# Kernel tuning notes

Hardware: AMD Instinct MI355X
Metric: run time of the kernel (lower is better)

The kernel has to match this reference:

```python
import jax, jax.numpy as jnp
import numpy as np
import math

D_MODEL = 512
N_HEADS = 4
ANCHOR_PERIODS = [12, 24, 48, 96]
MIN_PERIOD = 4


def compute_periods(x, k=2, min_period=MIN_PERIOD):
    # x: [B, T, C] -> per-channel top-k ACF periods [C, k] (torch code runs this under no_grad)
    B, T, C = x.shape
    xc = x - x.mean(axis=1, keepdims=True)
    n_fft = 1 << (2 * T - 1).bit_length()
    xf = jnp.fft.rfft(xc, n=n_fft, axis=1)
    acf = jnp.fft.irfft(xf * jnp.conj(xf), n=n_fft, axis=1)[:, :T, :]
    avg = acf.mean(axis=0)  # [T, C]
    neg = jnp.array(-jnp.inf, avg.dtype)
    avg = avg.at[:min_period, :].set(neg)
    prev = jnp.roll(avg, 1, axis=0)
    nxt = jnp.roll(avg, -1, axis=0)
    is_peak = (avg > prev) & (avg > nxt) & (avg > 0)
    masked = jnp.where(is_peak, avg, neg)
    _, inds = jax.lax.top_k(masked.T, k)  # [C, k], top over lag axis
    return jnp.clip(inds, min_period, T // 2)


def _interp_matrix(new_len, old_len):
    # rows of F.interpolate(eye, size=(new_len, old_len), mode='bilinear', align_corners=False)
    j = np.arange(new_len, dtype=np.float64)
    src = np.clip((j + 0.5) * old_len / new_len - 0.5, 0.0, old_len - 1)
    i0 = np.floor(src).astype(np.int64)
    i1 = np.minimum(i0 + 1, old_len - 1)
    w = src - i0
    M = np.zeros((new_len, old_len), np.float32)
    M[np.arange(new_len), i0] += (1.0 - w).astype(np.float32)
    M[np.arange(new_len), i1] += w.astype(np.float32)
    return M


def flex_weight(anchors, target_len):
    nearest = min(ANCHOR_PERIODS, key=lambda p: abs(p - target_len))
    old = anchors[nearest]  # [d, nearest]
    if nearest == target_len:
        return old
    M = _interp_matrix(target_len, nearest)          # [new, old]
    Mpinv = jnp.asarray(np.linalg.pinv(M.T))          # pinv(resize_mat.T): [new, old]
    return (Mpinv @ old.T).T * math.sqrt(target_len / nearest)  # [d, new]


def attentive_agg(tokens, in_w, in_b, out_w, out_b, ln_g, ln_b):
    # tokens: [N, P, d]; MHA(query=last patch, key=value=all patches), eval mode (dropout=identity)
    N, P, d = tokens.shape
    hd = d // N_HEADS
    q = tokens[:, -1:, :]  # [N, 1, d]
    Wq, Wk, Wv = jnp.split(in_w, 3, axis=0)
    bq, bk, bv = jnp.split(in_b, 3)

    def heads(t, W, b):
        y = t @ W.T + b
        return y.reshape(N, t.shape[1], N_HEADS, hd).transpose(0, 2, 1, 3)

    Q = heads(q, Wq, bq)       # [N, H, 1, hd]
    K = heads(tokens, Wk, bk)  # [N, H, P, hd]
    V = heads(tokens, Wv, bv)
    attn = jax.nn.softmax(jnp.einsum('nhqe,nhke->nhqk', Q, K) / math.sqrt(hd), axis=-1)
    o = jnp.einsum('nhqk,nhke->nhqe', attn, V).transpose(0, 2, 1, 3).reshape(N, 1, d)
    o = o @ out_w.T + out_b
    y = q + o
    mu = y.mean(-1, keepdims=True)
    var = y.var(-1, keepdims=True)
    y = (y - mu) * jax.lax.rsqrt(var + 1e-5) * ln_g + ln_b
    return y[:, 0, :]


def setup_inputs() -> dict:
    key = jax.random.key(0)
    ks = jax.random.split(key, 16)
    B, T, C, d = 16, 384, 128, D_MODEL

    def xavier(k, shape):
        lim = math.sqrt(6.0 / (shape[0] + shape[1]))
        return jax.random.uniform(k, shape, jnp.float32, -lim, lim)

    inp = {'x': jax.random.normal(ks[0], (B, T, C), jnp.float32)}
    for i, p in enumerate(ANCHOR_PERIODS):
        inp[f'anchor_w{p}'] = xavier(ks[1 + i], (d, p))
    inp['shared_bias'] = jnp.zeros((d,), jnp.float32)
    for j, tag in enumerate(['agg1', 'agg2']):
        inp[f'{tag}_in_w'] = xavier(ks[5 + 2 * j], (3 * d, d))
        inp[f'{tag}_in_b'] = jnp.zeros((3 * d,), jnp.float32)
        inp[f'{tag}_out_w'] = xavier(ks[6 + 2 * j], (d, d))
        inp[f'{tag}_out_b'] = jnp.zeros((d,), jnp.float32)
        inp[f'{tag}_ln_g'] = jnp.ones((d,), jnp.float32)
        inp[f'{tag}_ln_b'] = jnp.zeros((d,), jnp.float32)
    inp['fusion_w1'] = xavier(ks[9], (d, 3 * d))
    inp['fusion_b1'] = jnp.zeros((d,), jnp.float32)
    inp['fusion_w2'] = xavier(ks[10], (d, d))
    inp['fusion_b2'] = jnp.zeros((d,), jnp.float32)
    return inp


def reference(x, anchor_w12, anchor_w24, anchor_w48, anchor_w96, shared_bias,
              agg1_in_w, agg1_in_b, agg1_out_w, agg1_out_b, agg1_ln_g, agg1_ln_b,
              agg2_in_w, agg2_in_b, agg2_out_w, agg2_out_b, agg2_ln_g, agg2_ln_b,
              fusion_w1, fusion_b1, fusion_w2, fusion_b2):
    B, T, C = x.shape
    d = D_MODEL
    periods = np.asarray(jax.device_get(compute_periods(x)))  # [C, 2] (no-grad routing)
    anchors = {12: anchor_w12, 24: anchor_w24, 48: anchor_w48, 96: anchor_w96}
    x_inv = jnp.transpose(x, (0, 2, 1))  # [B, C, T]

    w_trend = flex_weight(anchors, T)
    trend = x_inv @ w_trend.T + shared_bias  # [B, C, d]

    s1 = jnp.zeros((B, C, d), x.dtype)
    s2 = jnp.zeros((B, C, d), x.dtype)
    agg1 = (agg1_in_w, agg1_in_b, agg1_out_w, agg1_out_b, agg1_ln_g, agg1_ln_b)
    agg2 = (agg2_in_w, agg2_in_b, agg2_out_w, agg2_out_b, agg2_ln_g, agg2_ln_b)

    for p in np.unique(periods):
        p = int(p)
        m1 = periods[:, 0] == p
        m2 = periods[:, 1] == p
        tgt_idx = np.where(m1 | m2)[0]
        if tgt_idx.size == 0:
            continue
        w_p = flex_weight(anchors, p)
        num_p = T // p
        # unfold(size=p, step=p) == contiguous reshape of the first num_p*p samples
        patches = x_inv[:, tgt_idx, :num_p * p].reshape(B, tgt_idx.size, num_p, p)
        tokens = patches @ w_p.T + shared_bias  # [B, Csub, num_p, d]
        for m, aggp, slot in ((m1, agg1, 0), (m2, agg2, 1)):
            idx = np.where(m)[0]
            if idx.size == 0:
                continue
            rel = np.isin(tgt_idx, idx)
            sub = tokens[:, rel].reshape(-1, num_p, d)
            res = attentive_agg(sub, *aggp).reshape(B, idx.size, d)
            if slot == 0:
                s1 = s1.at[:, idx, :].set(res)
            else:
                s2 = s2.at[:, idx, :].set(res)

    combined = jnp.concatenate([s1, s2, trend], axis=-1)  # [B, C, 3d]
    h = jax.nn.gelu(combined @ fusion_w1.T + fusion_b1, approximate=False)
    return h @ fusion_w2.T + fusion_b2  # [B, C, d] (final dropout = identity in eval)
```

## Files before the change

### kernel.cpp

```cpp
#include <hip/hip_runtime.h>
#include <math.h>

#define Bn 16
#define Tn 384
#define Cn 128

static constexpr long OFF_XT   = 0;
static constexpr long OFF_AVG  = 786432;
static constexpr long OFF_PER  = 835584;
static constexpr long OFF_MP   = 835840;
static constexpr long OFF_AT   = 2507140;
static constexpr long OFF_WAF  = 2605444;
static constexpr long OFF_QAT  = 3195268;
static constexpr long OFF_VAT  = 3391876;
static constexpr long OFF_OVT  = 3588484;
static constexpr long OFF_CON  = 4374916;
static constexpr long OFF_VB   = 4377988;
static constexpr long OFF_MT   = 4379012;
static constexpr long OFF_DEF  = 4673924;
static constexpr long OFF_COMB = 4677004;
static constexpr long OFF_H    = 7822732;
static constexpr long WS_FLOATS = 8871308;

__host__ __device__ inline int nanch(int p) {
  if (p == 384) return 96;
  return (p <= 18) ? 12 : (p <= 36) ? 24 : (p <= 72) ? 48 : 96;
}
__host__ __device__ inline int apre(int n) {
  return (n == 12) ? 0 : (n == 24) ? 12 : (n == 48) ? 36 : 84;
}
__host__ __device__ inline long mpoff(int p) {
  if (p == 384) return 1634436L;
  long T = (long)(p - 1) * p / 2;
  if (p <= 18) return 12 * (T - 6);
  if (p <= 36) return 1980 + 24 * (T - 171);
  if (p <= 72) return 13860 + 48 * (T - 666);
  return 108036 + 96 * (T - 2628);
}

__device__ inline void irow(int j, int newl, int oldl, int& i0, int& i1, float& w) {
  double src = ((double)j + 0.5) * (double)oldl / (double)newl - 0.5;
  if (src < 0.0) src = 0.0;
  double mx = (double)(oldl - 1);
  if (src > mx) src = mx;
  int a = (int)src;
  if (a > oldl - 1) a = oldl - 1;
  i0 = a;
  i1 = (a + 1 < oldl) ? (a + 1) : (oldl - 1);
  w = (float)(src - (double)a);
}

__global__ __launch_bounds__(256) void transpose_kernel(const float* __restrict__ x,
                                                        float* __restrict__ xT) {
  __shared__ float tile[32 * 129];
  int bid = blockIdx.x;
// ... 199 lines not shown
    for (int i = m - 2; i >= 0; --i) {
      float zi = (i >= j) ? ginv[i * 97 + j] : 0.f;
      xn = zi * idt[i] - cp[i] * xn;
      ginv[i * 97 + j] = xn;
    }
  }
  __syncthreads();
  if (p >= n) {
    for (int idx = tid; idx < p * n; idx += 256) {
      int t = idx / n, k = idx - t * n;
      int i0 = ii[t]; float w = ww[t];
      int i1 = min(i0 + 1, n - 1);
      dst[idx] = (1.f - w) * ginv[i0 * 97 + k] + w * ginv[i1 * 97 + k];
    }
  } else {
    for (int t = tid; t < p; t += 256) {
      for (int k = 0; k < n; ++k) outp[t * 97 + k] = 0.f;
      for (int j = 0; j < p; ++j) {
        float hv = ginv[t * 97 + j];
        int i0 = ii[j]; float w = ww[j];
        int i1 = min(i0 + 1, n - 1);
        outp[t * 97 + i0] += hv * (1.f - w);
        outp[t * 97 + i1] += hv * w;
      }
    }
    __syncthreads();
    for (int idx = tid; idx < p * n; idx += 256) {
      int t = idx / n, k = idx - t * n;
      dst[idx] = outp[t * 97 + k];
    }
  }
}

__global__ __launch_bounds__(256) void at_kernel(const float* __restrict__ a12,
                                                 const float* __restrict__ a24,
                                                 const float* __restrict__ a48,
                                                 const float* __restrict__ a96,
                                                 float* __restrict__ at_tab) {
  __shared__ float tile[64 * 97];
  int bid = blockIdx.x;
  int a = bid >> 3, d0 = (bid & 7) * 64;
  int n = (a == 0) ? 12 : (a == 1) ? 24 : (a == 2) ? 48 : 96;
  const float* src = (a == 0) ? a12 : (a == 1) ? a24 : (a == 2) ? a48 : a96;
  float* dst = at_tab + (long)apre(n) * 512;
  int tid = threadIdx.x;
  for (int i = tid; i < 64 * n; i += 256) {
    int dd = i / n, k = i - dd * n;
    tile[dd * 97 + k] = src[(long)(d0 + dd) * n + (long)k];
  }
  __syncthreads();
  for (int i = tid; i < n * 64; i += 256) {
    int k = i >> 6, dd = i & 63;
    dst[(long)k * 512 + d0 + dd] = tile[dd * 97 + k];
  }
  if (bid == 0) {
    for (int i = tid; i < 12 * 512; i += 256) at_tab[180L * 512 + i] = 0.f;
  }
}

__global__ __launch_bounds__(256) void constsA(const float* __restrict__ i1w,
                                               const float* __restrict__ i1b,
                                               const float* __restrict__ i2w,
                                               const float* __restrict__ i2b,
                                               const float* __restrict__ sb,
                                               float* __restrict__ cons,
                                               float* __restrict__ vbuf) {
  __shared__ float sv[512];
  int bid = blockIdx.x;
  int s = bid / 96, r0 = (bid % 96) * 16;
  const float* inw = s ? i2w : i1w;
  const float* inb = s ? i2b : i1b;
  int tid = threadIdx.x;
  for (int i = tid; i < 512; i += 256) sv[i] = sb[i];
  __syncthreads();
  int lane = tid & 63, w = tid >> 6;
  for (int rr = 0; rr < 4; ++rr) {
    int r = r0 + w * 4 + rr;
    const float* row = inw + (long)r * 512;
    float part = 0.f;
    for (int kk = 0; kk < 8; ++kk) part += row[lane + 64 * kk] * sv[lane + 64 * kk];
    for (int off = 32; off > 0; off >>= 1) part += __shfl_down(part, off, 64);
    if (lane == 0) {
      float v = part + inb[r];
      if (r < 1024) cons[s * 1536 + r] = v;
      else vbuf[s * 512 + (r - 1024)] = v;
    }
  }
}

__global__ __launch_bounds__(256) void constsB(const float* __restrict__ o1w,
                                               const float* __restrict__ o1b,
                                               const float* __restrict__ o2w,
                                               const float* __restrict__ o2b,
                                               const float* __restrict__ vbuf,
                                               float* __restrict__ cons) {
  __shared__ float vv[512];
  int bid = blockIdx.x;
  int s = bid / 32, r0 = (bid % 32) * 16;
  const float* outw = s ? o2w : o1w;
  const float* outb = s ? o2b : o1b;
  int tid = threadIdx.x;
  for (int i = tid; i < 512; i += 256) vv[i] = vbuf[s * 512 + i];
  __syncthreads();
  int lane = tid & 63, w = tid >> 6;
  for (int rr = 0; rr < 4; ++rr) {
    int r = r0 + w * 4 + rr;
    const float* row = outw + (long)r * 512;
    float part = 0.f;
    for (int kk = 0; kk < 8; ++kk) part += row[lane + 64 * kk] * vv[lane + 64 * kk];
    for (int off = 32; off > 0; off >>= 1) part += __shfl_down(part, off, 64);
    if (lane == 0) cons[s * 1536 + 1024 + r] = part + outb[r];
  }
}

__global__ __launch_bounds__(256) void wa_gemm2(const float* __restrict__ iw0,
                                                const float* __restrict__ iw1,
                                                const float* __restrict__ atb,
                                                float* __restrict__ waf,
                                                float* __restrict__ qat,
                                                float* __restrict__ vat) {
  __shared__ float smem[2 * 32 * 68];
  float* As = smem;
  float* Ws = smem + 32 * 68;
  int bid = blockIdx.x;
  int s = bid / 72, r = bid % 72;
  int m0 = (r / 3) * 64, n0 = (r % 3) * 64;
  const float* A = s ? iw1 : iw0;
  float* wafs = waf + (long)s * 294912;
  int tid = threadIdx.x;
  int tm = tid & 15, tn = tid >> 4;
  float acc[4][4];
#pragma unroll
  for (int i = 0; i < 4; ++i)
#pragma unroll
    for (int j = 0; j < 4; ++j) acc[i][j] = 0.f;
  int row = tid >> 3, kc = (tid & 7) * 4;
  for (int k0 = 0; k0 < 512; k0 += 32) {
    float4 v = *(const float4*)&A[(long)(m0 + row) * 512 + k0 + kc];
    As[(kc + 0) * 68 + row] = v.x; As[(kc + 1) * 68 + row] = v.y;
    As[(kc + 2) * 68 + row] = v.z; As[(kc + 3) * 68 + row] = v.w;
    v = *(const float4*)&A[(long)(m0 + row + 32) * 512 + k0 + kc];
    As[(kc + 0) * 68 + row + 32] = v.x; As[(kc + 1) * 68 + row + 32] = v.y;
    As[(kc + 2) * 68 + row + 32] = v.z; As[(kc + 3) * 68 + row + 32] = v.w;
    v = *(const float4*)&atb[(long)(n0 + row) * 512 + k0 + kc];
    Ws[(kc + 0) * 68 + row] = v.x; Ws[(kc + 1) * 68 + row] = v.y;
// ... 5 lines not shown
    for (int kk = 0; kk < 32; ++kk) {
      float4 a = *(const float4*)&As[kk * 68 + tm * 4];
      float4 w = *(const float4*)&Ws[kk * 68 + tn * 4];
      acc[0][0] += a.x * w.x; acc[0][1] += a.x * w.y; acc[0][2] += a.x * w.z; acc[0][3] += a.x * w.w;
      acc[1][0] += a.y * w.x; acc[1][1] += a.y * w.y; acc[1][2] += a.y * w.z; acc[1][3] += a.y * w.w;
      acc[2][0] += a.z * w.x; acc[2][1] += a.z * w.y; acc[2][2] += a.z * w.z; acc[2][3] += a.z * w.w;
      acc[3][0] += a.w * w.x; acc[3][1] += a.w * w.y; acc[3][2] += a.w * w.z; acc[3][3] += a.w * w.w;
    }
    __syncthreads();
  }
#pragma unroll
  for (int mi = 0; mi < 4; ++mi) {
    float4 o;
    o.x = acc[mi][0]; o.y = acc[mi][1]; o.z = acc[mi][2]; o.w = acc[mi][3];
    *(float4*)&wafs[(long)(m0 + tm * 4 + mi) * 192 + n0 + tn * 4] = o;
  }
  if (m0 < 512 || m0 >= 1024) {
    float* Ct = smem;
#pragma unroll
    for (int mi = 0; mi < 4; ++mi)
#pragma unroll
      for (int j = 0; j < 4; ++j)
        Ct[(tn * 4 + j) * 65 + tm * 4 + mi] = acc[mi][j];
    __syncthreads();
    float* dst = ((m0 < 512) ? qat : vat) + (long)s * 98304;
    int mr = m0 & 511;
    for (int i = tid; i < 64 * 64; i += 256) {
      int cc = i >> 6, rr = i & 63;
      dst[(long)(n0 + cc) * 512 + mr + rr] = Ct[cc * 65 + rr];
    }
  }
}

__global__ __launch_bounds__(256) void mt_gemm(const float* __restrict__ qat,
                                               const float* __restrict__ waf,
                                               float* __restrict__ mt) {
  __shared__ float As[32 * 68];
  __shared__ float Ws[32 * 68];
  int bid = blockIdx.x;
  int s4h = bid / 9, t = bid % 9;
  int s = s4h >> 2, h = s4h & 3;
  int m0 = (t / 3) * 64, n0 = (t % 3) * 64;
  const float* A = qat + (long)s * 98304 + h * 128;
  const float* B = waf + (long)s * 294912 + 98304 + (long)(h * 128) * 192;
  float* C = mt + (long)s4h * 36864;
  int tid = threadIdx.x;
  int tm = tid & 15, tn = tid >> 4;
  float acc[4][4];
#pragma unroll
  for (int i = 0; i < 4; ++i)
#pragma unroll
    for (int j = 0; j < 4; ++j) acc[i][j] = 0.f;
  int row = tid >> 3, kc = (tid & 7) * 4;
  for (int k0 = 0; k0 < 128; k0 += 32) {
    float4 v = *(const float4*)&A[(long)(m0 + row) * 512 + k0 + kc];
    As[(kc + 0) * 68 + row] = v.x; As[(kc + 1) * 68 + row] = v.y;
    As[(kc + 2) * 68 + row] = v.z; As[(kc + 3) * 68 + row] = v.w;
    v = *(const float4*)&A[(long)(m0 + row + 32) * 512 + k0 + kc];
    As[(kc + 0) * 68 + row + 32] = v.x; As[(kc + 1) * 68 + row + 32] = v.y;
    As[(kc + 2) * 68 + row + 32] = v.z; As[(kc + 3) * 68 + row + 32] = v.w;
    for (int l = tid; l < 512; l += 256) {
      int i = l >> 4, kq = (l & 15) * 4;
      float4 b = *(const float4*)&B[(long)(k0 + i) * 192 + n0 + kq];
      Ws[i * 68 + kq + 0] = b.x; Ws[i * 68 + kq + 1] = b.y;
      Ws[i * 68 + kq + 2] = b.z; Ws[i * 68 + kq + 3] = b.w;
    }
    __syncthreads();
    for (int kk = 0; kk < 32; ++kk) {
      float4 a = *(const float4*)&As[kk * 68 + tm * 4];
      float4 w = *(const float4*)&Ws[kk * 68 + tn * 4];
      acc[0][0] += a.x * w.x; acc[0][1] += a.x * w.y; acc[0][2] += a.x * w.z; acc[0][3] += a.x * w.w;
      acc[1][0] += a.y * w.x; acc[1][1] += a.y * w.y; acc[1][2] += a.y * w.z; acc[1][3] += a.y * w.w;
      acc[2][0] += a.z * w.x; acc[2][1] += a.z * w.y; acc[2][2] += a.z * w.z; acc[2][3] += a.z * w.w;
      acc[3][0] += a.w * w.x; acc[3][1] += a.w * w.y; acc[3][2] += a.w * w.z; acc[3][3] += a.w * w.w;
    }
    __syncthreads();
  }
#pragma unroll
  for (int mi = 0; mi < 4; ++mi) {
    float4 o;
    o.x = acc[mi][0]; o.y = acc[mi][1]; o.z = acc[mi][2]; o.w = acc[mi][3];
    *(float4*)&C[(long)(m0 + tm * 4 + mi) * 192 + n0 + tn * 4] = o;
  }
}

__global__ __launch_bounds__(256) void scoreconsts(const float* __restrict__ qat,
                                                   const float* __restrict__ waf,
                                                   const float* __restrict__ cons,
                                                   float* __restrict__ def) {
  __shared__ float qcl[128];
  __shared__ float kbl[128];
  int bid = blockIdx.x;
  int s = bid >> 2, h = bid & 3;
  int tid = threadIdx.x;
  const float* qc = cons + s * 1536;
  const float* kb = qc + 512;
  if (tid < 128) {
    qcl[tid] = qc[h * 128 + tid];
    kbl[tid] = kb[h * 128 + tid];
  }
  __syncthreads();
  const float* katb = waf + (long)s * 294912 + 98304;
  const float* qats = qat + (long)s * 98304;
  float* dtab = def + (long)(s * 4 + h) * 192;
  float* etab = def + 1536 + (long)(s * 4 + h) * 192;
  float* ftab = def + 3072 + (s * 4 + h);
  if (tid < 192) {
    float acc = 0.f;
    for (int i = 0; i < 128; ++i) acc += katb[(long)(h * 128 + i) * 192 + tid] * qcl[i];
    dtab[tid] = acc;
    float acc2 = 0.f;
    const float* qr = qats + (long)tid * 512 + h * 128;
    for (int i = 0; i < 128; ++i) acc2 += qr[i] * kbl[i];
    etab[tid] = acc2;
  }
  if (tid < 64) {
    float acc = 0.f;
    for (int i = tid; i < 128; i += 64) acc += qcl[i] * kbl[i];
    for (int off = 32; off > 0; off >>= 1) acc += __shfl_down(acc, off, 64);
    if (tid == 0) *ftab = acc;
  }
}

__global__ __launch_bounds__(256) void ova_gemm2(const float* __restrict__ ow0,
                                                 const float* __restrict__ ow1,
                                                 const float* __restrict__ vat,
                                                 float* __restrict__ ovt) {
  __shared__ float As[32 * 68];
  __shared__ float Ws[32 * 68];
  int bid = blockIdx.x;
  int s = bid / 96, r = bid % 96;
  int h = r / 24, r2 = r % 24;
  int m0 = (r2 / 8) * 64, n0 = (r2 % 8) * 64;
  const float* A = vat + (long)s * 98304 + h * 128;
  const float* W = (s ? ow1 : ow0) + h * 128;
  float* C = ovt + ((long)(s * 4 + h) * 192) * 512;
  int tid = threadIdx.x;
  int tm = tid & 15, tn = tid >> 4;
  float acc[4][4];
#pragma unroll
  for (int i = 0; i < 4; ++i)
#pragma unroll
    for (int j = 0; j < 4; ++j) acc[i][j] = 0.f;
  int row = tid >> 3, kc = (tid & 7) * 4;
  for (int k0 = 0; k0 < 128; k0 += 32) {
    float4 v = *(const float4*)&A[(long)(m0 + row) * 512 + k0 + kc];
    As[(kc + 0) * 68 + row] = v.x; As[(kc + 1) * 68 + row] = v.y;
    As[(kc + 2) * 68 + row] = v.z; As[(kc + 3) * 68 + row] = v.w;
    v = *(const float4*)&A[(long)(m0 + row + 32) * 512 + k0 + kc];
    As[(kc + 0) * 68 + row + 32] = v.x; As[(kc + 1) * 68 + row + 32] = v.y;
    As[(kc + 2) * 68 + row + 32] = v.z; As[(kc + 3) * 68 + row + 32] = v.w;
    v = *(const float4*)&W[(long)(n0 + row) * 512 + k0 + kc];
    Ws[(kc + 0) * 68 + row] = v.x; Ws[(kc + 1) * 68 + row] = v.y;
    Ws[(kc + 2) * 68 + row] = v.z; Ws[(kc + 3) * 68 + row] = v.w;
    v = *(const float4*)&W[(long)(n0 + row + 32) * 512 + k0 + kc];
    Ws[(kc + 0) * 68 + row + 32] = v.x; Ws[(kc + 1) * 68 + row + 32] = v.y;
    Ws[(kc + 2) * 68 + row + 32] = v.z; Ws[(kc + 3) * 68 + row + 32] = v.w;
    __syncthreads();
    for (int kk = 0; kk < 32; ++kk) {
      float4 a = *(const float4*)&As[kk * 68 + tm * 4];
      float4 w = *(const float4*)&Ws[kk * 68 + tn * 4];
      acc[0][0] += a.x * w.x; acc[0][1] += a.x * w.y; acc[0][2] += a.x * w.z; acc[0][3] += a.x * w.w;
      acc[1][0] += a.y * w.x; acc[1][1] += a.y * w.y; acc[1][2] += a.y * w.z; acc[1][3] += a.y * w.w;
      acc[2][0] += a.z * w.x; acc[2][1] += a.z * w.y; acc[2][2] += a.z * w.z; acc[2][3] += a.z * w.w;
      acc[3][0] += a.w * w.x; acc[3][1] += a.w * w.y; acc[3][2] += a.w * w.z; acc[3][3] += a.w * w.w;
    }
    __syncthreads();
  }
#pragma unroll
  for (int mi = 0; mi < 4; ++mi) {
    float4 o;
    o.x = acc[mi][0]; o.y = acc[mi][1]; o.z = acc[mi][2]; o.w = acc[mi][3];
    *(float4*)&C[(long)(m0 + tm * 4 + mi) * 512 + n0 + tn * 4] = o;
  }
}

__global__ __launch_bounds__(256) void attn_kernel(
    const float* __restrict__ xT, const int* __restrict__ per,
    const float* __restrict__ mp, const float* __restrict__ mt,
    const float* __restrict__ def, const float* __restrict__ ovt,
    const float* __restrict__ cons, const float* __restrict__ at_tab,
    const float* __restrict__ sb,
    const float* __restrict__ l1g, const float* __restrict__ l1b,
    const float* __restrict__ l2g, const float* __restrict__ l2b,
    float* __restrict__ comb) {
  __shared__ float xb[8 * 384];
  __shared__ float Z[8 * 1248];
  __shared__ float zl[8 * 96];
  __shared__ float arb[8 * 384];
  __shared__ float qkc[32];
  __shared__ float red[4 * 16];
  __shared__ float stats[16];
  float* scp = xb;

  int tid = threadIdx.x;
  int bid = blockIdx.x;
  int slot = bid & 1;
  int c = (bid >> 1) & 127;
  int b0 = (bid >> 8) * 8;
  int p = per[c * 2 + slot];
  int n = nanch(p);
  int np = Tn / p;
  int n1 = n + 1;
  float s = sqrtf((float)p / (float)n);
  float s2 = s * s;
  const float rscale = 0.08838834764831845f;
  int pre = apre(n);
  const float* mpp = mp + mpoff(p);
  const float* atb = at_tab + (long)pre * 512;
  const float* oc = cons + slot * 1536 + 1024;
  const float* lng = slot ? l2g : l1g;
  const float* lnb = slot ? l2b : l1b;
  const float* dt = def + (long)(slot * 4) * 192;
  const float* et = def + 1536 + (long)(slot * 4) * 192;
  const float* ft = def + 3072 + slot * 4;
  const float* mtb = mt + (long)(slot * 4) * 36864;

  for (int g = 0; g < 8; ++g)
    for (int t = tid; t < Tn; t += 256)
      xb[g * 384 + t] = xT[((long)c * Bn + b0 + g) * Tn + t];
  __syncthreads();

  int znp = np * n;
  for (int idx = tid; idx < znp; idx += 256) {
    int j = idx / n, k = idx - j * n;
    int jb = j * p;
    const float* mk = mpp + k;
    float a[8];
#pragma unroll
    for (int g = 0; g < 8; ++g) a[g] = 0.f;
    for (int t = 0; t < p; ++t) {
      float m = mk[(long)t * n];
#pragma unroll
      for (int g = 0; g < 8; ++g) a[g] += m * xb[g * 384 + jb + t];
    }
    int zi = j * n1 + k;
#pragma unroll
    for (int g = 0; g < 8; ++g) Z[g * 1248 + zi] = a[g];
  }
  __syncthreads();

  for (int idx = tid; idx < 8 * n; idx += 256) {
    int g = idx / n, k = idx - g * n;
    zl[g * 96 + k] = Z[g * 1248 + (np - 1) * n1 + k];
  }
  __syncthreads();

  {
    int pair = tid >> 3, l = tid & 7;
    int g = pair >> 2, h = pair & 3;
    const float* eh = et + h * 192 + pre;
    float acc = 0.f;
    for (int j = l; j < n; j += 8) acc += eh[j] * zl[g * 96 + j];
    for (int off = 4; off > 0; off >>= 1) acc += __shfl_down(acc, off, 8);
    if (l == 0) qkc[g * 4 + h] = s * acc + ft[h];
  }
  {
    int tot = 4 * n;
    for (int idx = tid; idx < tot; idx += 256) {
      int h = idx / n, k = idx - h * n;
      const float* mtc = mtb + (long)h * 36864 + (long)pre * 192 + pre + k;
      float a[8];
#pragma unroll
      for (int g = 0; g < 8; ++g) a[g] = 0.f;
      for (int j0 = 0; j0 < n; j0 += 4) {
        float4 zb[8];
#pragma unroll
        for (int g = 0; g < 8; ++g) zb[g] = *(const float4*)&zl[g * 96 + j0];
#pragma unroll
        for (int c4 = 0; c4 < 4; ++c4) {
          float mv = mtc[(long)(j0 + c4) * 192];
// ... 29 lines not shown

  {
    int pair = tid >> 3, l = tid & 7;
    int g = pair >> 2, h = pair & 3;
    float* sp = scp + g * 384 + h * np;
    float m = -1e30f;
    for (int j = l; j < np; j += 8) m = fmaxf(m, sp[j]);
    for (int off = 4; off > 0; off >>= 1) m = fmaxf(m, __shfl_xor(m, off, 8));
    float lsum = 0.f;
    for (int j = l; j < np; j += 8) { float e = expf(sp[j] - m); sp[j] = e; lsum += e; }
    for (int off = 4; off > 0; off >>= 1) lsum += __shfl_xor(lsum, off, 8);
    float il = 1.f / lsum;
    for (int j = l; j < np; j += 8) sp[j] *= il;
  }
  __syncthreads();

  {
    int fn = 4 * n;
    int tot = 8 * fn;
    for (int idx = tid; idx < tot; idx += 256) {
      int g = idx / fn;
      int r = idx - g * fn;
      int h = r / n, k = r - h * n;
      const float* sp = scp + g * 384 + h * np;
      const float* zp = Z + g * 1248 + k;
      float acc = 0.f;
      for (int j = 0; j < np; ++j) acc += sp[j] * zp[j * n1];
      arb[g * 384 + h * 96 + k] = acc;
    }
  }
  __syncthreads();

  {
    int d0 = 2 * tid;
    float a0[8], a1[8];
#pragma unroll
    for (int g = 0; g < 8; ++g) { a0[g] = 0.f; a1[g] = 0.f; }
    for (int k0 = 0; k0 < n; k0 += 4) {
      float4 zb[8];
#pragma unroll
      for (int g = 0; g < 8; ++g) zb[g] = *(const float4*)&zl[g * 96 + k0];
#pragma unroll
      for (int c4 = 0; c4 < 4; ++c4) {
        float2 w = *(const float2*)&atb[(long)(k0 + c4) * 512 + d0];
#pragma unroll
        for (int g = 0; g < 8; ++g) {
          float zv = (c4 == 0) ? zb[g].x : (c4 == 1) ? zb[g].y : (c4 == 2) ? zb[g].z : zb[g].w;
          a0[g] += w.x * zv; a1[g] += w.y * zv;
        }
      }
    }
    for (int h = 0; h < 4; ++h) {
      const float* op = ovt + ((long)((slot * 4 + h) * 192 + pre)) * 512;
      const float* zhb = arb + h * 96;
      for (int k0 = 0; k0 < n; k0 += 4) {
        float4 zb[8];
#pragma unroll
        for (int g = 0; g < 8; ++g) zb[g] = *(const float4*)&zhb[g * 384 + k0];
#pragma unroll
        for (int c4 = 0; c4 < 4; ++c4) {
          float2 w = *(const float2*)&op[(long)(k0 + c4) * 512 + d0];
#pragma unroll
          for (int g = 0; g < 8; ++g) {
            float zv = (c4 == 0) ? zb[g].x : (c4 == 1) ? zb[g].y : (c4 == 2) ? zb[g].z : zb[g].w;
            a0[g] += w.x * zv; a1[g] += w.y * zv;
          }
        }
      }
    }
    float2 sbv = *(const float2*)&sb[d0];
    float2 ocv = *(const float2*)&oc[d0];
    float s0 = sbv.x + ocv.x, s1v = sbv.y + ocv.y;
#pragma unroll
    for (int g = 0; g < 8; ++g) { a0[g] = s * a0[g] + s0; a1[g] = s * a1[g] + s1v; }
    float ps[16];
#pragma unroll
    for (int g = 0; g < 8; ++g) {
      ps[2 * g] = a0[g] + a1[g];
      ps[2 * g + 1] = a0[g] * a0[g] + a1[g] * a1[g];
    }
    int w = tid >> 6, lane = tid & 63;
    for (int off = 32; off > 0; off >>= 1) {
#pragma unroll
      for (int i = 0; i < 16; ++i) ps[i] += __shfl_down(ps[i], off, 64);
    }
    if (lane == 0) {
#pragma unroll
      for (int i = 0; i < 16; ++i) red[w * 16 + i] = ps[i];
    }
    __syncthreads();
    if (tid < 8) {
      int g = tid;
      float ssum = red[2 * g] + red[16 + 2 * g] + red[32 + 2 * g] + red[48 + 2 * g];
      float qsum = red[2 * g + 1] + red[16 + 2 * g + 1] + red[32 + 2 * g + 1] + red[48 + 2 * g + 1];
      float mu = ssum / 512.f;
      float var = qsum / 512.f - mu * mu;
      stats[g * 2] = mu;
      stats[g * 2 + 1] = rsqrtf(var + 1e-5f);
    }
    __syncthreads();
    float2 gv = *(const float2*)&lng[d0];
    float2 bv = *(const float2*)&lnb[d0];
#pragma unroll
    for (int g = 0; g < 8; ++g) {
      float mu = stats[g * 2], rstd = stats[g * 2 + 1];
      long base = ((long)(b0 + g) * Cn + c) * 1536 + slot * 512;
      float2 o;
      o.x = (a0[g] - mu) * rstd * gv.x + bv.x;
      o.y = (a1[g] - mu) * rstd * gv.y + bv.y;
      *(float2*)&comb[base + d0] = o;
    }
  }
}

__global__ __launch_bounds__(256) void trend_kernel(const float* __restrict__ xT,
                                                    const float* __restrict__ mp384,
                                                    const float* __restrict__ at96,
                                                    const float* __restrict__ sb,
                                                    float* __restrict__ comb) {
  __shared__ float xb[Bn * Tn];
  __shared__ float Ztr[Bn * 97];
  int c = blockIdx.x, tid = threadIdx.x;
  for (int i = tid; i < Bn * Tn; i += 256) xb[i] = xT[(long)c * Bn * Tn + i];
  __syncthreads();
  for (int idx = tid; idx < 4 * 96; idx += 256) {
    int bq = idx / 96, k = idx - bq * 96;
    const float* x0 = xb + (bq * 4 + 0) * Tn;
    const float* x1 = xb + (bq * 4 + 1) * Tn;
    const float* x2 = xb + (bq * 4 + 2) * Tn;
    const float* x3 = xb + (bq * 4 + 3) * Tn;
    const float* mk = mp384 + k;
    float a0 = 0.f, a1 = 0.f, a2 = 0.f, a3 = 0.f;
    for (int t = 0; t < Tn; ++t) {
      float m = mk[(long)t * 96];
      a0 += m * x0[t]; a1 += m * x1[t]; a2 += m * x2[t]; a3 += m * x3[t];
    }
    Ztr[(bq * 4 + 0) * 97 + k] = a0;
    Ztr[(bq * 4 + 1) * 97 + k] = a1;
    Ztr[(bq * 4 + 2) * 97 + k] = a2;
    Ztr[(bq * 4 + 3) * 97 + k] = a3;
  }
  __syncthreads();
  float acc0[Bn], acc1[Bn];
#pragma unroll
  for (int b = 0; b < Bn; ++b) { acc0[b] = 0.f; acc1[b] = 0.f; }
  for (int k = 0; k < 96; ++k) {
    float w0 = at96[(long)k * 512 + tid];
    float w1 = at96[(long)k * 512 + 256 + tid];
#pragma unroll
    for (int b = 0; b < Bn; ++b) {
      float z = Ztr[b * 97 + k];
      acc0[b] += w0 * z;
      acc1[b] += w1 * z;
    }
  }
  float s0 = sb[tid], s1 = sb[256 + tid];
#pragma unroll
  for (int b = 0; b < Bn; ++b) {
    long base = ((long)b * Cn + c) * 1536 + 1024;
    comb[base + tid] = 2.f * acc0[b] + s0;
    comb[base + 256 + tid] = 2.f * acc1[b] + s1;
  }
}

template <bool GELU>
__global__ __launch_bounds__(256) void fused_gemm(const float* __restrict__ A,
                                                  const float* __restrict__ W,
                                                  const float* __restrict__ bias,
                                                  float* __restrict__ C,
                                                  int N, int K) {
  __shared__ float As[32 * 68];
  __shared__ float Ws[32 * 68];
  int nb = N >> 6;
  int m0 = (blockIdx.x / nb) * 64, n0 = (blockIdx.x % nb) * 64;
  int tid = threadIdx.x;
  int tm = tid & 15, tn = tid >> 4;
  float acc[4][4];
#pragma unroll
  for (int i = 0; i < 4; ++i)
#pragma unroll
    for (int j = 0; j < 4; ++j) acc[i][j] = 0.f;
  int row = tid >> 3, kc = (tid & 7) * 4;
  for (int k0 = 0; k0 < K; k0 += 32) {
    {
      float4 v = *(const float4*)&A[(long)(m0 + row) * K + k0 + kc];
      As[(kc + 0) * 68 + row] = v.x; As[(kc + 1) * 68 + row] = v.y;
      As[(kc + 2) * 68 + row] = v.z; As[(kc + 3) * 68 + row] = v.w;
      v = *(const float4*)&A[(long)(m0 + row + 32) * K + k0 + kc];
      As[(kc + 0) * 68 + row + 32] = v.x; As[(kc + 1) * 68 + row + 32] = v.y;
      As[(kc + 2) * 68 + row + 32] = v.z; As[(kc + 3) * 68 + row + 32] = v.w;
      v = *(const float4*)&W[(long)(n0 + row) * K + k0 + kc];
      Ws[(kc + 0) * 68 + row] = v.x; Ws[(kc + 1) * 68 + row] = v.y;
      Ws[(kc + 2) * 68 + row] = v.z; Ws[(kc + 3) * 68 + row] = v.w;
      v = *(const float4*)&W[(long)(n0 + row + 32) * K + k0 + kc];
      Ws[(kc + 0) * 68 + row + 32] = v.x; Ws[(kc + 1) * 68 + row + 32] = v.y;
// ... 39 lines not shown
  const float* g1iw = (const float*)d_in[6];
  const float* g1ib = (const float*)d_in[7];
  const float* g1ow = (const float*)d_in[8];
  const float* g1ob = (const float*)d_in[9];
  const float* g1lg = (const float*)d_in[10];
  const float* g1lb = (const float*)d_in[11];
  const float* g2iw = (const float*)d_in[12];
  const float* g2ib = (const float*)d_in[13];
  const float* g2ow = (const float*)d_in[14];
  const float* g2ob = (const float*)d_in[15];
  const float* g2lg = (const float*)d_in[16];
  const float* g2lb = (const float*)d_in[17];
  const float* fw1  = (const float*)d_in[18];
  const float* fb1  = (const float*)d_in[19];
  const float* fw2  = (const float*)d_in[20];
  const float* fb2  = (const float*)d_in[21];

  if (ws_size < (size_t)WS_FLOATS * sizeof(float)) return;

  float* ws   = (float*)d_ws;
  float* xT   = ws + OFF_XT;
  float* avg  = ws + OFF_AVG;
  int*   per  = (int*)(ws + OFF_PER);
  float* mp   = ws + OFF_MP;
  float* atb  = ws + OFF_AT;
  float* waf  = ws + OFF_WAF;
  float* qat  = ws + OFF_QAT;
  float* vat  = ws + OFF_VAT;
  float* ovt  = ws + OFF_OVT;
  float* cons = ws + OFF_CON;
  float* vbuf = ws + OFF_VB;
  float* mtab = ws + OFF_MT;
  float* def  = ws + OFF_DEF;
  float* comb = ws + OFF_COMB;
  float* hbuf = ws + OFF_H;
  float* out  = (float*)d_out;

  transpose_kernel<<<192, 256, 0, stream>>>(x, xT);
  acf_kernel<<<Cn * 6, 256, 0, stream>>>(xT, avg);
  periods_kernel<<<32, 256, 0, stream>>>(avg, per);
  build_mpinv_kernel<<<190, 256, 0, stream>>>(per, mp);
  at_kernel<<<32, 256, 0, stream>>>(a12, a24, a48, a96, atb);
  constsA<<<192, 256, 0, stream>>>(g1iw, g1ib, g2iw, g2ib, sb, cons, vbuf);
  constsB<<<64, 256, 0, stream>>>(g1ow, g1ob, g2ow, g2ob, vbuf, cons);
  wa_gemm2<<<144, 256, 0, stream>>>(g1iw, g2iw, atb, waf, qat, vat);
  mt_gemm<<<72, 256, 0, stream>>>(qat, waf, mtab);
  scoreconsts<<<8, 256, 0, stream>>>(qat, waf, cons, def);
  ova_gemm2<<<192, 256, 0, stream>>>(g1ow, g2ow, vat, ovt);

  attn_kernel<<<512, 256, 0, stream>>>(xT, per, mp, mtab, def, ovt, cons, atb, sb,
                                       g1lg, g1lb, g2lg, g2lb, comb);
  trend_kernel<<<Cn, 256, 0, stream>>>(xT, mp + 1634436L, atb + 84L * 512, sb, comb);
  fused_gemm<true><<<256, 256, 0, stream>>>(comb, fw1, fb1, hbuf, 512, 1536);
  fused_gemm<false><<<256, 256, 0, stream>>>(hbuf, fw2, fb2, out, 512, 512);
}
```

Measured before the change: 447.1 us.

## Merge prep kernels, split attention into two stages, split-K the first fusion GEMM

Several small weight-preprocessing kernels are combined into two multi-role launches (prep1, prep2) to cut launch count and idle time between them. The attention kernel is split in two: attn_a writes per-row scaled coefficient vectors to a workspace buffer, and attn_y applies the output projection to 16 batch rows per block, so each weight row is reused across more rows. The Z projection in attn_a now reads two matrix columns at a time with float2 loads. The 1536-wide fusion GEMM is split along K into two halves for more blocks, followed by a separate bias+GELU reduction kernel. This costs extra workspace traffic and more launches.

```diff
diff --git a/kernel.cpp b/kernel.cpp
--- a/kernel.cpp
+++ b/kernel.cpp
@@ -18,9 +18,11 @@
 static constexpr long OFF_VB   = 4377988;
 static constexpr long OFF_MT   = 4379012;
 static constexpr long OFF_DEF  = 4673924;
-static constexpr long OFF_COMB = 4677004;
-static constexpr long OFF_H    = 7822732;
-static constexpr long WS_FLOATS = 8871308;
+static constexpr long OFF_ZC   = 4677004;
+static constexpr long OFF_COMB = 6643084;
+static constexpr long OFF_H    = 9788812;
+static constexpr long OFF_H2   = 10837388;
+static constexpr long WS_FLOATS = 11885964;
 
 __host__ __device__ inline int nanch(int p) {
   if (p == 384) return 96;
@@ -286,13 +288,10 @@
   }
 }
 
-__global__ __launch_bounds__(256) void at_kernel(const float* __restrict__ a12,
-                                                 const float* __restrict__ a24,
-                                                 const float* __restrict__ a48,
-                                                 const float* __restrict__ a96,
-                                                 float* __restrict__ at_tab) {
-  __shared__ float tile[64 * 97];
-  int bid = blockIdx.x;
+__device__ void at_body(int bid, const float* __restrict__ a12,
+                        const float* __restrict__ a24, const float* __restrict__ a48,
+                        const float* __restrict__ a96, float* __restrict__ at_tab,
+                        float* tile) {
   int a = bid >> 3, d0 = (bid & 7) * 64;
   int n = (a == 0) ? 12 : (a == 1) ? 24 : (a == 2) ? 48 : 96;
   const float* src = (a == 0) ? a12 : (a == 1) ? a24 : (a == 2) ? a48 : a96;
@@ -312,15 +311,11 @@
   }
 }
 
-__global__ __launch_bounds__(256) void constsA(const float* __restrict__ i1w,
-                                               const float* __restrict__ i1b,
-                                               const float* __restrict__ i2w,
-                                               const float* __restrict__ i2b,
-                                               const float* __restrict__ sb,
-                                               float* __restrict__ cons,
-                                               float* __restrict__ vbuf) {
-  __shared__ float sv[512];
-  int bid = blockIdx.x;
+__device__ void constsA_body(int bid, const float* __restrict__ i1w,
+                             const float* __restrict__ i1b, const float* __restrict__ i2w,
+                             const float* __restrict__ i2b, const float* __restrict__ sb,
+                             float* __restrict__ cons, float* __restrict__ vbuf,
+                             float* sv) {
   int s = bid / 96, r0 = (bid % 96) * 16;
   const float* inw = s ? i2w : i1w;
   const float* inb = s ? i2b : i1b;
@@ -342,29 +337,22 @@
   }
 }
 
-__global__ __launch_bounds__(256) void constsB(const float* __restrict__ o1w,
-                                               const float* __restrict__ o1b,
-                                               const float* __restrict__ o2w,
-                                               const float* __restrict__ o2b,
-                                               const float* __restrict__ vbuf,
-                                               float* __restrict__ cons) {
-  __shared__ float vv[512];
+__global__ __launch_bounds__(256) void prep1(const float* __restrict__ a12,
+                                             const float* __restrict__ a24,
+                                             const float* __restrict__ a48,
+                                             const float* __restrict__ a96,
+                                             const float* __restrict__ i1w,
+                                             const float* __restrict__ i1b,
+                                             const float* __restrict__ i2w,
+                                             const float* __restrict__ i2b,
+                                             const float* __restrict__ sb,
+                                             float* __restrict__ at_tab,
+                                             float* __restrict__ cons,
+                                             float* __restrict__ vbuf) {
+  __shared__ float sm[64 * 97];
   int bid = blockIdx.x;
-  int s = bid / 32, r0 = (bid % 32) * 16;
-  const float* outw = s ? o2w : o1w;
-  const float* outb = s ? o2b : o1b;
-  int tid = threadIdx.x;
-  for (int i = tid; i < 512; i += 256) vv[i] = vbuf[s * 512 + i];
-  __syncthreads();
-  int lane = tid & 63, w = tid >> 6;
-  for (int rr = 0; rr < 4; ++rr) {
-    int r = r0 + w * 4 + rr;
-    const float* row = outw + (long)r * 512;
-    float part = 0.f;
-    for (int kk = 0; kk < 8; ++kk) part += row[lane + 64 * kk] * vv[lane + 64 * kk];
-    for (int off = 32; off > 0; off >>= 1) part += __shfl_down(part, off, 64);
-    if (lane == 0) cons[s * 1536 + 1024 + r] = part + outb[r];
-  }
+  if (bid < 32) at_body(bid, a12, a24, a48, a96, at_tab, sm);
+  else constsA_body(bid - 32, i1w, i1b, i2w, i2b, sb, cons, vbuf, sm);
 }
 
 __global__ __launch_bounds__(256) void wa_gemm2(const float* __restrict__ iw0,
@@ -436,12 +424,30 @@
   }
 }
 
-__global__ __launch_bounds__(256) void mt_gemm(const float* __restrict__ qat,
-                                               const float* __restrict__ waf,
-                                               float* __restrict__ mt) {
-  __shared__ float As[32 * 68];
-  __shared__ float Ws[32 * 68];
-  int bid = blockIdx.x;
+__device__ void constsB_body(int bid, const float* __restrict__ o1w,
+                             const float* __restrict__ o1b, const float* __restrict__ o2w,
+                             const float* __restrict__ o2b, const float* __restrict__ vbuf,
+                             float* __restrict__ cons, float* vv) {
+  int s = bid / 32, r0 = (bid % 32) * 16;
+  const float* outw = s ? o2w : o1w;
+  const float* outb = s ? o2b : o1b;
+  int tid = threadIdx.x;
+  for (int i = tid; i < 512; i += 256) vv[i] = vbuf[s * 512 + i];
+  __syncthreads();
+  int lane = tid & 63, w = tid >> 6;
+  for (int rr = 0; rr < 4; ++rr) {
+    int r = r0 + w * 4 + rr;
+    const float* row = outw + (long)r * 512;
+    float part = 0.f;
+    for (int kk = 0; kk < 8; ++kk) part += row[lane + 64 * kk] * vv[lane + 64 * kk];
+    for (int off = 32; off > 0; off >>= 1) part += __shfl_down(part, off, 64);
+    if (lane == 0) cons[s * 1536 + 1024 + r] = part + outb[r];
+  }
+}
+
+__device__ void mt_body(int bid, const float* __restrict__ qat,
+                        const float* __restrict__ waf, float* __restrict__ mt,
+                        float* As, float* Ws) {
   int s4h = bid / 9, t = bid % 9;
   int s = s4h >> 2, h = s4h & 3;
   int m0 = (t / 3) * 64, n0 = (t % 3) * 64;
@@ -488,13 +494,9 @@
   }
 }
 
-__global__ __launch_bounds__(256) void scoreconsts(const float* __restrict__ qat,
-                                                   const float* __restrict__ waf,
-                                                   const float* __restrict__ cons,
-                                                   float* __restrict__ def) {
-  __shared__ float qcl[128];
-  __shared__ float kbl[128];
-  int bid = blockIdx.x;
+__device__ void sc_body(int bid, const float* __restrict__ qat,
+                        const float* __restrict__ waf, const float* __restrict__ cons,
+                        float* __restrict__ def, float* qcl, float* kbl) {
   int s = bid >> 2, h = bid & 3;
   int tid = threadIdx.x;
   const float* qc = cons + s * 1536;
@@ -526,13 +528,9 @@
   }
 }
 
-__global__ __launch_bounds__(256) void ova_gemm2(const float* __restrict__ ow0,
-                                                 const float* __restrict__ ow1,
-                                                 const float* __restrict__ vat,
-                                                 float* __restrict__ ovt) {
-  __shared__ float As[32 * 68];
-  __shared__ float Ws[32 * 68];
-  int bid = blockIdx.x;
+__device__ void ova_body(int bid, const float* __restrict__ ow0,
+                         const float* __restrict__ ow1, const float* __restrict__ vat,
+                         float* __restrict__ ovt, float* As, float* Ws) {
   int s = bid / 96, r = bid % 96;
   int h = r / 24, r2 = r % 24;
   int m0 = (r2 / 8) * 64, n0 = (r2 % 8) * 64;
@@ -579,22 +577,35 @@
   }
 }
 
-__global__ __launch_bounds__(256) void attn_kernel(
+__global__ __launch_bounds__(256) void prep2(const float* __restrict__ o1w,
+                                             const float* __restrict__ o1b,
+                                             const float* __restrict__ o2w,
+                                             const float* __restrict__ o2b,
+                                             const float* __restrict__ vbuf,
+                                             float* __restrict__ cons,
+                                             const float* __restrict__ qat,
+                                             const float* __restrict__ waf,
+                                             float* __restrict__ mtab,
+                                             float* __restrict__ def,
+                                             const float* __restrict__ vat,
+                                             float* __restrict__ ovt) {
+  __shared__ float sm[2 * 32 * 68];
+  int bid = blockIdx.x;
+  if (bid < 64) constsB_body(bid, o1w, o1b, o2w, o2b, vbuf, cons, sm);
+  else if (bid < 136) mt_body(bid - 64, qat, waf, mtab, sm, sm + 32 * 68);
+  else if (bid < 144) sc_body(bid - 136, qat, waf, cons, def, sm, sm + 128);
+  else ova_body(bid - 144, o1w, o2w, vat, ovt, sm, sm + 32 * 68);
+}
+
+__global__ __launch_bounds__(256) void attn_a(
     const float* __restrict__ xT, const int* __restrict__ per,
     const float* __restrict__ mp, const float* __restrict__ mt,
-    const float* __restrict__ def, const float* __restrict__ ovt,
-    const float* __restrict__ cons, const float* __restrict__ at_tab,
-    const float* __restrict__ sb,
-    const float* __restrict__ l1g, const float* __restrict__ l1b,
-    const float* __restrict__ l2g, const float* __restrict__ l2b,
-    float* __restrict__ comb) {
+    const float* __restrict__ def, float* __restrict__ zc) {
   __shared__ float xb[8 * 384];
   __shared__ float Z[8 * 1248];
   __shared__ float zl[8 * 96];
   __shared__ float arb[8 * 384];
   __shared__ float qkc[32];
-  __shared__ float red[4 * 16];
-  __shared__ float stats[16];
   float* scp = xb;
 
   int tid = threadIdx.x;
@@ -611,10 +622,6 @@
   const float rscale = 0.08838834764831845f;
   int pre = apre(n);
   const float* mpp = mp + mpoff(p);
-  const float* atb = at_tab + (long)pre * 512;
-  const float* oc = cons + slot * 1536 + 1024;
-  const float* lng = slot ? l2g : l1g;
-  const float* lnb = slot ? l2b : l1b;
   const float* dt = def + (long)(slot * 4) * 192;
   const float* et = def + 1536 + (long)(slot * 4) * 192;
   const float* ft = def + 3072 + slot * 4;
@@ -625,22 +632,33 @@
       xb[g * 384 + t] = xT[((long)c * Bn + b0 + g) * Tn + t];
   __syncthreads();
 
-  int znp = np * n;
-  for (int idx = tid; idx < znp; idx += 256) {
-    int j = idx / n, k = idx - j * n;
-    int jb = j * p;
-    const float* mk = mpp + k;
-    float a[8];
-#pragma unroll
-    for (int g = 0; g < 8; ++g) a[g] = 0.f;
-    for (int t = 0; t < p; ++t) {
-      float m = mk[(long)t * n];
-#pragma unroll
-      for (int g = 0; g < 8; ++g) a[g] += m * xb[g * 384 + jb + t];
-    }
-    int zi = j * n1 + k;
-#pragma unroll
-    for (int g = 0; g < 8; ++g) Z[g * 1248 + zi] = a[g];
+  {
+    int half = n >> 1;
+    int tot1 = np * half;
+    for (int idx = tid; idx < tot1; idx += 256) {
+      int j = idx / half, k2 = idx - j * half;
+      int k = k2 * 2;
+      int jb = j * p;
+      const float* mk = mpp + k;
+      float a0[8], a1[8];
+#pragma unroll
+      for (int g = 0; g < 8; ++g) { a0[g] = 0.f; a1[g] = 0.f; }
+      for (int t = 0; t < p; ++t) {
+        float2 m = *(const float2*)&mk[(long)t * n];
+#pragma unroll
+        for (int g = 0; g < 8; ++g) {
+          float xv = xb[g * 384 + jb + t];
+          a0[g] += m.x * xv;
+          a1[g] += m.y * xv;
+        }
+      }
+      int zi = j * n1 + k;
+#pragma unroll
+      for (int g = 0; g < 8; ++g) {
+        Z[g * 1248 + zi] = a0[g];
+        Z[g * 1248 + zi + 1] = a1[g];
+      }
+    }
   }
   __syncthreads();
 
@@ -736,84 +754,111 @@
   __syncthreads();
 
   {
-    int d0 = 2 * tid;
-    float a0[8], a1[8];
-#pragma unroll
-    for (int g = 0; g < 8; ++g) { a0[g] = 0.f; a1[g] = 0.f; }
+    long rowb = ((long)slot * 128 + c) * 16 + b0;
+    int fn5 = 5 * n;
+    int tot = 8 * fn5;
+    for (int idx = tid; idx < tot; idx += 256) {
+      int g = idx / fn5, r = idx - g * fn5;
+      int seg = r / n, k = r - seg * n;
+      float v = (seg == 0) ? zl[g * 96 + k] : arb[g * 384 + (seg - 1) * 96 + k];
+      zc[(rowb + g) * 480 + seg * 96 + k] = s * v;
+    }
+  }
+}
+
+__global__ __launch_bounds__(256) void attn_y(
+    const int* __restrict__ per, const float* __restrict__ zc,
+    const float* __restrict__ at_tab, const float* __restrict__ ovt,
+    const float* __restrict__ cons, const float* __restrict__ sb,
+    const float* __restrict__ l1g, const float* __restrict__ l1b,
+    const float* __restrict__ l2g, const float* __restrict__ l2b,
+    float* __restrict__ comb) {
+  __shared__ float zbuf[16 * 480];
+  __shared__ float red[128];
+  __shared__ float stats[32];
+  int tid = threadIdx.x;
+  int bid = blockIdx.x;
+  int slot = bid & 1, c = bid >> 1;
+  int p = per[c * 2 + slot];
+  int n = nanch(p);
+  int pre = apre(n);
+  const float* atb = at_tab + (long)pre * 512;
+  const float* oc = cons + slot * 1536 + 1024;
+  const float* lng = slot ? l2g : l1g;
+  const float* lnb = slot ? l2b : l1b;
+  long rowb = ((long)slot * 128 + c) * 16;
+  int fn5 = 5 * n;
+  for (int idx = tid; idx < 16 * fn5; idx += 256) {
+    int g = idx / fn5, r = idx - g * fn5;
+    int seg = r / n, k = r - seg * n;
+    zbuf[g * 480 + seg * 96 + k] = zc[(rowb + g) * 480 + seg * 96 + k];
+  }
+  __syncthreads();
+  int d0 = 2 * tid;
+  float acc0[16], acc1[16];
+#pragma unroll
+  for (int r = 0; r < 16; ++r) { acc0[r] = 0.f; acc1[r] = 0.f; }
+  for (int seg = 0; seg < 5; ++seg) {
+    const float* wt = (seg == 0) ? atb
+                                 : (ovt + ((long)(slot * 4 + seg - 1) * 192 + pre) * 512);
+    int zoff = seg * 96;
     for (int k0 = 0; k0 < n; k0 += 4) {
-      float4 zb[8];
-#pragma unroll
-      for (int g = 0; g < 8; ++g) zb[g] = *(const float4*)&zl[g * 96 + k0];
+      float4 zv[16];
+#pragma unroll
+      for (int r = 0; r < 16; ++r) zv[r] = *(const float4*)&zbuf[r * 480 + zoff + k0];
 #pragma unroll
       for (int c4 = 0; c4 < 4; ++c4) {
-        float2 w = *(const float2*)&atb[(long)(k0 + c4) * 512 + d0];
-#pragma unroll
-        for (int g = 0; g < 8; ++g) {
-          float zv = (c4 == 0) ? zb[g].x : (c4 == 1) ? zb[g].y : (c4 == 2) ? zb[g].z : zb[g].w;
-          a0[g] += w.x * zv; a1[g] += w.y * zv;
+        float2 w = *(const float2*)&wt[(long)(k0 + c4) * 512 + d0];
+#pragma unroll
+        for (int r = 0; r < 16; ++r) {
+          float z = (c4 == 0) ? zv[r].x : (c4 == 1) ? zv[r].y : (c4 == 2) ? zv[r].z : zv[r].w;
+          acc0[r] += w.x * z;
+          acc1[r] += w.y * z;
         }
       }
     }
-    for (int h = 0; h < 4; ++h) {
-      const float* op = ovt + ((long)((slot * 4 + h) * 192 + pre)) * 512;
-      const float* zhb = arb + h * 96;
-      for (int k0 = 0; k0 < n; k0 += 4) {
-        float4 zb[8];
-#pragma unroll
-        for (int g = 0; g < 8; ++g) zb[g] = *(const float4*)&zhb[g * 384 + k0];
-#pragma unroll
-        for (int c4 = 0; c4 < 4; ++c4) {
-          float2 w = *(const float2*)&op[(long)(k0 + c4) * 512 + d0];
-#pragma unroll
-          for (int g = 0; g < 8; ++g) {
-            float zv = (c4 == 0) ? zb[g].x : (c4 == 1) ? zb[g].y : (c4 == 2) ? zb[g].z : zb[g].w;
-            a0[g] += w.x * zv; a1[g] += w.y * zv;
-          }
-        }
-      }
-    }
-    float2 sbv = *(const float2*)&sb[d0];
-    float2 ocv = *(const float2*)&oc[d0];
-    float s0 = sbv.x + ocv.x, s1v = sbv.y + ocv.y;
-#pragma unroll
-    for (int g = 0; g < 8; ++g) { a0[g] = s * a0[g] + s0; a1[g] = s * a1[g] + s1v; }
-    float ps[16];
-#pragma unroll
-    for (int g = 0; g < 8; ++g) {
-      ps[2 * g] = a0[g] + a1[g];
-      ps[2 * g + 1] = a0[g] * a0[g] + a1[g] * a1[g];
-    }
-    int w = tid >> 6, lane = tid & 63;
-    for (int off = 32; off > 0; off >>= 1) {
-#pragma unroll
-      for (int i = 0; i < 16; ++i) ps[i] += __shfl_down(ps[i], off, 64);
-    }
-    if (lane == 0) {
-#pragma unroll
-      for (int i = 0; i < 16; ++i) red[w * 16 + i] = ps[i];
-    }
-    __syncthreads();
-    if (tid < 8) {
-      int g = tid;
-      float ssum = red[2 * g] + red[16 + 2 * g] + red[32 + 2 * g] + red[48 + 2 * g];
-      float qsum = red[2 * g + 1] + red[16 + 2 * g + 1] + red[32 + 2 * g + 1] + red[48 + 2 * g + 1];
-      float mu = ssum / 512.f;
-      float var = qsum / 512.f - mu * mu;
-      stats[g * 2] = mu;
-      stats[g * 2 + 1] = rsqrtf(var + 1e-5f);
-    }
-    __syncthreads();
-    float2 gv = *(const float2*)&lng[d0];
-    float2 bv = *(const float2*)&lnb[d0];
-#pragma unroll
-    for (int g = 0; g < 8; ++g) {
-      float mu = stats[g * 2], rstd = stats[g * 2 + 1];
-      long base = ((long)(b0 + g) * Cn + c) * 1536 + slot * 512;
-      float2 o;
-      o.x = (a0[g] - mu) * rstd * gv.x + bv.x;
-      o.y = (a1[g] - mu) * rstd * gv.y + bv.y;
-      *(float2*)&comb[base + d0] = o;
-    }
+  }
+  float2 sbv = *(const float2*)&sb[d0];
+  float2 ocv = *(const float2*)&oc[d0];
+  float s0 = sbv.x + ocv.x, s1 = sbv.y + ocv.y;
+#pragma unroll
+  for (int r = 0; r < 16; ++r) { acc0[r] += s0; acc1[r] += s1; }
+  float ps[32];
+#pragma unroll
+  for (int r = 0; r < 16; ++r) {
+    ps[2 * r] = acc0[r] + acc1[r];
+    ps[2 * r + 1] = acc0[r] * acc0[r] + acc1[r] * acc1[r];
+  }
+  int w = tid >> 6, lane = tid & 63;
+  for (int off = 32; off > 0; off >>= 1) {
+#pragma unroll
+    for (int i = 0; i < 32; ++i) ps[i] += __shfl_down(ps[i], off, 64);
+  }
+  if (lane == 0) {
+#pragma unroll
+    for (int i = 0; i < 32; ++i) red[w * 32 + i] = ps[i];
+  }
+  __syncthreads();
+  if (tid < 16) {
+    int r = tid;
+    float ssum = red[2 * r] + red[32 + 2 * r] + red[64 + 2 * r] + red[96 + 2 * r];
+    float qsum = red[2 * r + 1] + red[32 + 2 * r + 1] + red[64 + 2 * r + 1] + red[96 + 2 * r + 1];
+    float mu = ssum / 512.f;
+    float var = qsum / 512.f - mu * mu;
+    stats[2 * r] = mu;
+    stats[2 * r + 1] = rsqrtf(var + 1e-5f);
+  }
+  __syncthreads();
+  float2 gv = *(const float2*)&lng[d0];
+  float2 bv = *(const float2*)&lnb[d0];
+#pragma unroll
+  for (int r = 0; r < 16; ++r) {
+    float mu = stats[2 * r], rstd = stats[2 * r + 1];
+    long base = ((long)r * Cn + c) * 1536 + slot * 512;
+    float2 o;
+    o.x = (acc0[r] - mu) * rstd * gv.x + bv.x;
+    o.y = (acc1[r] - mu) * rstd * gv.y + bv.y;
+    *(float2*)&comb[base + d0] = o;
   }
 }
 
@@ -865,6 +910,79 @@
     comb[base + tid] = 2.f * acc0[b] + s0;
     comb[base + 256 + tid] = 2.f * acc1[b] + s1;
   }
+}
+
+__global__ __launch_bounds__(256) void gemm1_part(const float* __restrict__ A,
+                                                  const float* __restrict__ W,
+                                                  float* __restrict__ C0,
+                                                  float* __restrict__ C1) {
+  __shared__ float As[32 * 68];
+  __shared__ float Ws[32 * 68];
+  int bid = blockIdx.x;
+  int kh = bid >> 8;
+  int r = bid & 255;
+  int m0 = (r >> 3) * 64, n0 = (r & 7) * 64;
+  float* C = kh ? C1 : C0;
+  const float* Ab = A + kh * 768;
+  const float* Wb = W + kh * 768;
+  int tid = threadIdx.x;
+  int tm = tid & 15, tn = tid >> 4;
+  float acc[4][4];
+#pragma unroll
+  for (int i = 0; i < 4; ++i)
+#pragma unroll
+    for (int j = 0; j < 4; ++j) acc[i][j] = 0.f;
+  int row = tid >> 3, kc = (tid & 7) * 4;
+  for (int k0 = 0; k0 < 768; k0 += 32) {
+    float4 v = *(const float4*)&Ab[(long)(m0 + row) * 1536 + k0 + kc];
+    As[(kc + 0) * 68 + row] = v.x; As[(kc + 1) * 68 + row] = v.y;
+    As[(kc + 2) * 68 + row] = v.z; As[(kc + 3) * 68 + row] = v.w;
+    v = *(const float4*)&Ab[(long)(m0 + row + 32) * 1536 + k0 + kc];
+    As[(kc + 0) * 68 + row + 32] = v.x; As[(kc + 1) * 68 + row + 32] = v.y;
+    As[(kc + 2) * 68 + row + 32] = v.z; As[(kc + 3) * 68 + row + 32] = v.w;
+    v = *(const float4*)&Wb[(long)(n0 + row) * 1536 + k0 + kc];
+    Ws[(kc + 0) * 68 + row] = v.x; Ws[(kc + 1) * 68 + row] = v.y;
+    Ws[(kc + 2) * 68 + row] = v.z; Ws[(kc + 3) * 68 + row] = v.w;
+    v = *(const float4*)&Wb[(long)(n0 + row + 32) * 1536 + k0 + kc];
+    Ws[(kc + 0) * 68 + row + 32] = v.x; Ws[(kc + 1) * 68 + row + 32] = v.y;
+    Ws[(kc + 2) * 68 + row + 32] = v.z; Ws[(kc + 3) * 68 + row + 32] = v.w;
+    __syncthreads();
+    for (int kk = 0; kk < 32; ++kk) {
+      float4 a = *(const float4*)&As[kk * 68 + tm * 4];
+      float4 w = *(const float4*)&Ws[kk * 68 + tn * 4];
+      acc[0][0] += a.x * w.x; acc[0][1] += a.x * w.y; acc[0][2] += a.x * w.z; acc[0][3] += a.x * w.w;
+      acc[1][0] += a.y * w.x; acc[1][1] += a.y * w.y; acc[1][2] += a.y * w.z; acc[1][3] += a.y * w.w;
+      acc[2][0] += a.z * w.x; acc[2][1] += a.z * w.y; acc[2][2] += a.z * w.z; acc[2][3] += a.z * w.w;
+      acc[3][0] += a.w * w.x; acc[3][1] += a.w * w.y; acc[3][2] += a.w * w.z; acc[3][3] += a.w * w.w;
+    }
+    __syncthreads();
+  }
+#pragma unroll
+  for (int mi = 0; mi < 4; ++mi) {
+    float4 o;
+    o.x = acc[mi][0]; o.y = acc[mi][1]; o.z = acc[mi][2]; o.w = acc[mi][3];
+    *(float4*)&C[(long)(m0 + tm * 4 + mi) * 512 + n0 + tn * 4] = o;
+  }
+}
+
+__global__ __launch_bounds__(256) void gelu_red(float* __restrict__ H,
+                                                const float* __restrict__ H2,
+                                                const float* __restrict__ fb1) {
+  int i = blockIdx.x * 256 + threadIdx.x;
+  float4 a = ((const float4*)H)[i];
+  float4 b = ((const float4*)H2)[i];
+  int col4 = (i & 127) << 2;
+  float4 bs = *(const float4*)&fb1[col4];
+  float4 v;
+  v.x = a.x + b.x + bs.x;
+  v.y = a.y + b.y + bs.y;
+  v.z = a.z + b.z + bs.z;
+  v.w = a.w + b.w + bs.w;
+  v.x = 0.5f * v.x * (1.f + erff(v.x * 0.7071067811865475f));
+  v.y = 0.5f * v.y * (1.f + erff(v.y * 0.7071067811865475f));
+  v.z = 0.5f * v.z * (1.f + erff(v.z * 0.7071067811865475f));
+  v.w = 0.5f * v.w * (1.f + erff(v.w * 0.7071067811865475f));
+  ((float4*)H)[i] = v;
 }
 
 template <bool GELU>
@@ -970,25 +1088,26 @@
   float* vbuf = ws + OFF_VB;
   float* mtab = ws + OFF_MT;
   float* def  = ws + OFF_DEF;
+  float* zc   = ws + OFF_ZC;
   float* comb = ws + OFF_COMB;
   float* hbuf = ws + OFF_H;
+  float* hbu2 = ws + OFF_H2;
   float* out  = (float*)d_out;
 
   transpose_kernel<<<192, 256, 0, stream>>>(x, xT);
   acf_kernel<<<Cn * 6, 256, 0, stream>>>(xT, avg);
   periods_kernel<<<32, 256, 0, stream>>>(avg, per);
   build_mpinv_kernel<<<190, 256, 0, stream>>>(per, mp);
-  at_kernel<<<32, 256, 0, stream>>>(a12, a24, a48, a96, atb);
-  constsA<<<192, 256, 0, stream>>>(g1iw, g1ib, g2iw, g2ib, sb, cons, vbuf);
-  constsB<<<64, 256, 0, stream>>>(g1ow, g1ob, g2ow, g2ob, vbuf, cons);
+  prep1<<<224, 256, 0, stream>>>(a12, a24, a48, a96, g1iw, g1ib, g2iw, g2ib, sb,
+                                 atb, cons, vbuf);
   wa_gemm2<<<144, 256, 0, stream>>>(g1iw, g2iw, atb, waf, qat, vat);
-  mt_gemm<<<72, 256, 0, stream>>>(qat, waf, mtab);
-  scoreconsts<<<8, 256, 0, stream>>>(qat, waf, cons, def);
-  ova_gemm2<<<192, 256, 0, stream>>>(g1ow, g2ow, vat, ovt);
-
-  attn_kernel<<<512, 256, 0, stream>>>(xT, per, mp, mtab, def, ovt, cons, atb, sb,
-                                       g1lg, g1lb, g2lg, g2lb, comb);
+  prep2<<<336, 256, 0, stream>>>(g1ow, g1ob, g2ow, g2ob, vbuf, cons,
+                                 qat, waf, mtab, def, vat, ovt);
+  attn_a<<<512, 256, 0, stream>>>(xT, per, mp, mtab, def, zc);
+  attn_y<<<256, 256, 0, stream>>>(per, zc, atb, ovt, cons, sb,
+                                  g1lg, g1lb, g2lg, g2lb, comb);
   trend_kernel<<<Cn, 256, 0, stream>>>(xT, mp + 1634436L, atb + 84L * 512, sb, comb);
-  fused_gemm<true><<<256, 256, 0, stream>>>(comb, fw1, fb1, hbuf, 512, 1536);
+  gemm1_part<<<512, 256, 0, stream>>>(comb, fw1, hbuf, hbu2);
+  gelu_red<<<1024, 256, 0, stream>>>(hbuf, hbu2, fb1);
   fused_gemm<false><<<256, 256, 0, stream>>>(hbuf, fw2, fb2, out, 512, 512);
 }
```

After: 440.7 us. About the same (-1.4%).
